# Kernel optimization log

Measured on AMD Instinct MI355X. Metric: run time of the kernel, lower is better.

## Reference

```python
import jax, jax.numpy as jnp
import numpy as np

B, S, D, H = 4, 2048, 1024, 16
HS = D // H  # head_size = 64


def setup_inputs() -> dict:
    key = jax.random.key(0)
    ks = jax.random.split(key, 6)
    scale = 1.0 / np.sqrt(D)
    return {
        "x": jax.random.normal(ks[0], (B, S, D), dtype=jnp.float32),
        "Wk": jax.random.normal(ks[1], (D, D), dtype=jnp.float32) * scale,
        "Wq": jax.random.normal(ks[2], (D, D), dtype=jnp.float32) * scale,
        "Wv": jax.random.normal(ks[3], (D, D), dtype=jnp.float32) * scale,
        "Wo": jax.random.normal(ks[4], (D, D), dtype=jnp.float32) * scale,
        "bo": jnp.zeros((D,), dtype=jnp.float32),
    }


def reference(x, Wk, Wq, Wv, Wo, bo):
    b, s, d = x.shape
    # torch nn.Linear: y = x @ W.T
    def heads(W):
        return (x @ W.T).reshape(b, s, H, HS).transpose(0, 2, 1, 3)  # [b,h,s,hs]
    k, q, v = heads(Wk), heads(Wq), heads(Wv)
    att = jnp.einsum("bhqd,bhkd->bhqk", q, k) * (1.0 / np.sqrt(HS))
    causal = jnp.tril(jnp.ones((s, s), dtype=bool))
    att = jnp.where(causal, att, -jnp.inf)
    att = jax.nn.softmax(att, axis=-1)
    # dropout in eval mode (identity) for deterministic reference
    out = jnp.einsum("bhqk,bhkd->bhqd", att, v)  # [b,h,s,hs]
    out = out.transpose(0, 2, 1, 3).reshape(b, s, d)
    return out @ Wo.T + bo
```

## Files before the change

kernel.cpp:

```cpp
#include <hip/hip_runtime.h>

#define B_ 4
#define S_ 2048
#define D_ 1024
#define H_ 16
#define HS_ 64

typedef float f32x4 __attribute__((ext_vector_type(4)));
typedef short bf16x8 __attribute__((ext_vector_type(8)));

__device__ inline short f2bf(float f) {
  union { float f; unsigned u; } v; v.f = f;
  unsigned r = v.u + 0x7fffu + ((v.u >> 16) & 1u);
  return (short)(r >> 16);
}
__device__ inline unsigned fbits(float f) {
  union { float f; unsigned u; } v; v.f = f; return v.u;
}

__device__ inline void load_lds16(const short* g, short* l) {
  __builtin_amdgcn_global_load_lds((const __attribute__((address_space(1))) void*)g,
                                   (__attribute__((address_space(3))) void*)l, 16, 0, 0);
}

__global__ __launch_bounds__(256) void cvt_f32_bf16(const float* __restrict__ in,
                                                    short* __restrict__ out, int n) {
  const int i = (blockIdx.x * 256 + threadIdx.x) * 4;
  if (i < n) {
    const float4 v = *(const float4*)(in + i);
    short4 o;
    o.x = f2bf(v.x); o.y = f2bf(v.y); o.z = f2bf(v.z); o.w = f2bf(v.w);
    *(short4*)(out + i) = o;
  }
}

__global__ __launch_bounds__(256) void cvt4_f32_bf16(const float* __restrict__ w0, const float* __restrict__ w1,
                                                     const float* __restrict__ w2, const float* __restrict__ w3,
                                                     short* __restrict__ o0, short* __restrict__ o1,
                                                     short* __restrict__ o2, short* __restrict__ o3, int n) {
  const float* in; short* out;
  switch (blockIdx.y) {
    case 0: in = w0; out = o0; break;
    case 1: in = w1; out = o1; break;
    case 2: in = w2; out = o2; break;
    default: in = w3; out = o3; break;
  }
  const int i = (blockIdx.x * 256 + threadIdx.x) * 4;
  if (i < n) {
    const float4 v = *(const float4*)(in + i);
    short4 o;
    o.x = f2bf(v.x); o.y = f2bf(v.y); o.z = f2bf(v.z); o.w = f2bf(v.w);
    *(short4*)(out + i) = o;
  }
}

__device__ inline void stage_tile64(const short* __restrict__ g, int ld, int k0,
                                    short* l, int tid) {
  const int srow = tid >> 3;
  const int scol = (tid & 7) * 8;
  const int scg  = ((tid & 7) ^ ((tid >> 3) & 7)) * 8;
  for (int j = 0; j < 4; j++)
    load_lds16(&g[(size_t)(srow + j * 32) * ld + k0 + scg], &l[(srow + j * 32) * 64 + scol]);
}

__device__ inline void mfma_core64(const short* lA, const short* lB, int wm, int wn,
                                   int col, int quad, f32x4 acc[4][4]) {
  for (int ks = 0; ks < 2; ks++) {
    const int cs = ((ks * 4 + quad) ^ (col & 7)) * 8;
    bf16x8 af[4], bfr[4];
    for (int i = 0; i < 4; i++) af[i]  = *(const bf16x8*)&lA[(wm + i * 16 + col) * 64 + cs];
    for (int j = 0; j < 4; j++) bfr[j] = *(const bf16x8*)&lB[(wn + j * 16 + col) * 64 + cs];
    for (int i = 0; i < 4; i++)
      for (int j = 0; j < 4; j++)
        acc[i][j] = __builtin_amdgcn_mfma_f32_16x16x32_bf16(af[i], bfr[j], acc[i][j], 0, 0, 0);
  }
}

template <bool CF32>
__global__ __launch_bounds__(256) void gemm_bb(const short* __restrict__ A,
                                               const short* __restrict__ Bt,
                                               void* __restrict__ Cv,
                                               const float* __restrict__ bias,
                                               int M, int N, int K) {
  __shared__ __align__(16) short lA[2][128 * 64];
  __shared__ __align__(16) short lB[2][128 * 64];
  const int tid = threadIdx.x;
  const int wave = tid >> 6, lane = tid & 63;
  const int quad = lane >> 4, col = lane & 15;
  const int m0 = blockIdx.x * 128, n0 = blockIdx.y * 128;
  const int wm = (wave >> 1) * 64, wn = (wave & 1) * 64;

  f32x4 acc[4][4];
  for (int i = 0; i < 4; i++)
    for (int j = 0; j < 4; j++) acc[i][j] = (f32x4){0.f, 0.f, 0.f, 0.f};

  const int NT = K >> 6;
  stage_tile64(&A[(size_t)m0 * K], K, 0, lA[0], tid);
  stage_tile64(&Bt[(size_t)n0 * K], K, 0, lB[0], tid);
  __syncthreads();
  for (int kt = 0; kt < NT; kt++) {
    const int cur = kt & 1;
    if (kt + 1 < NT) {
      stage_tile64(&A[(size_t)m0 * K], K, (kt + 1) * 64, lA[cur ^ 1], tid);
      stage_tile64(&Bt[(size_t)n0 * K], K, (kt + 1) * 64, lB[cur ^ 1], tid);
    }
    mfma_core64(lA[cur], lB[cur], wm, wn, col, quad, acc);
    __syncthreads();
  }

  for (int j = 0; j < 4; j++) {
    const int gn = n0 + wn + j * 16 + col;
    const float bv = bias ? bias[gn] : 0.f;
    for (int i = 0; i < 4; i++) {
      const int gm = m0 + wm + i * 16 + quad * 4;
      for (int r = 0; r < 4; r++) {
        if (CF32) ((float*)Cv)[(size_t)(gm + r) * N + gn] = acc[i][j][r] + bv;
        else      ((short*)Cv)[(size_t)(gm + r) * N + gn] = f2bf(acc[i][j][r] + bv);
      }
    }
  }
}

__global__ __launch_bounds__(512, 2) void gemm_qkv8(const short* __restrict__ A,
                                                    const short* Wq, const short* Wk, const short* Wv,
                                                    short* Cq, short* Ck, short* Cvt) {
  __shared__ __align__(16) short lds[3][24576];
  const int tid = threadIdx.x;
  const int wave = tid >> 6, lane = tid & 63;
  const int quad = lane >> 4, col = lane & 15;
  const int nsel = blockIdx.y >> 2;
  const int n0 = (blockIdx.y & 3) * 256;
  const short* Bt = nsel == 0 ? Wq : (nsel == 1 ? Wk : Wv);
  const int m0 = blockIdx.x * 128;
  const int wm = (wave >> 2) * 64, wn = (wave & 3) * 64;
  const int K = D_;
  const int NT = 16;

  const int srow = tid >> 3;
  const int sc8 = tid & 7;
  const short* gA = &A[(size_t)m0 * K];
  const short* gB = &Bt[(size_t)n0 * K];

  auto stageA = [&](int t, int p) {
    const int row = p * 64 + srow;
    load_lds16(&gA[(size_t)row * K + t * 64 + ((sc8 ^ (row & 7)) * 8)],
               &lds[t % 3][row * 64 + sc8 * 8]);
  };
  auto stageB = [&](int t, int p) {
    const int row = p * 64 + srow;
    load_lds16(&gB[(size_t)row * K + t * 64 + ((sc8 ^ (row & 7)) * 8)],
               &lds[t % 3][8192 + row * 64 + sc8 * 8]);
  };

  f32x4 acc[4][4];
#pragma unroll
  for (int i = 0; i < 4; i++)
#pragma unroll
    for (int j = 0; j < 4; j++) acc[i][j] = (f32x4){0.f, 0.f, 0.f, 0.f};

  stageA(0, 0); stageA(0, 1);
  for (int p = 0; p < 4; p++) stageB(0, p);
  stageA(1, 0); stageA(1, 1);
  for (int p = 0; p < 4; p++) stageB(1, p);
  asm volatile("s_waitcnt vmcnt(6)" ::: "memory");
  __builtin_amdgcn_sched_barrier(0);
  __builtin_amdgcn_s_barrier();

  for (int t = 0; t < NT; t++) {
    const short* la = lds[t % 3];
    const short* lb = la + 8192;

    bf16x8 bfr[4][2];
    {
      bf16x8 af[2][2];
#pragma unroll
      for (int j = 0; j < 4; j++)
#pragma unroll
        for (int kk = 0; kk < 2; kk++)
          bfr[j][kk] = *(const bf16x8*)&lb[(wn + j * 16 + col) * 64 +
                                           (((kk * 4 + quad) ^ (col & 7)) * 8)];
#pragma unroll
      for (int f = 0; f < 2; f++)
#pragma unroll
        for (int kk = 0; kk < 2; kk++)
          af[f][kk] = *(const bf16x8*)&la[(wm + f * 16 + col) * 64 +
                                          (((kk * 4 + quad) ^ (col & 7)) * 8)];
      if (t + 2 < NT) { stageB(t + 2, 0); stageB(t + 2, 1); stageB(t + 2, 2); }
      __builtin_amdgcn_sched_barrier(0);
      __builtin_amdgcn_s_barrier();
      asm volatile("s_waitcnt lgkmcnt(0)" ::: "memory");
      __builtin_amdgcn_sched_barrier(0);
      __builtin_amdgcn_s_setprio(1);
#pragma unroll
      for (int f = 0; f < 2; f++)
#pragma unroll
        for (int j = 0; j < 4; j++)
#pragma unroll
          for (int kk = 0; kk < 2; kk++)
            acc[f][j] = __builtin_amdgcn_mfma_f32_16x16x32_bf16(
                af[f][kk], bfr[j][kk], acc[f][j], 0, 0, 0);
      __builtin_amdgcn_s_setprio(0);
      __builtin_amdgcn_sched_barrier(0);
      __builtin_amdgcn_s_barrier();
    }
    {
      bf16x8 af[2][2];
#pragma unroll
      for (int f = 0; f < 2; f++)
#pragma unroll
        for (int kk = 0; kk < 2; kk++)
          af[f][kk] = *(const bf16x8*)&la[(wm + (2 + f) * 16 + col) * 64 +
                                          (((kk * 4 + quad) ^ (col & 7)) * 8)];
      if (t + 2 < NT) { stageB(t + 2, 3); stageA(t + 2, 0); stageA(t + 2, 1); }
      __builtin_amdgcn_sched_barrier(0);
      __builtin_amdgcn_s_barrier();
      asm volatile("s_waitcnt lgkmcnt(0)" ::: "memory");
      __builtin_amdgcn_sched_barrier(0);
      __builtin_amdgcn_s_setprio(1);
#pragma unroll
      for (int f = 0; f < 2; f++)
#pragma unroll
        for (int j = 0; j < 4; j++)
#pragma unroll
          for (int kk = 0; kk < 2; kk++)
            acc[2 + f][j] = __builtin_amdgcn_mfma_f32_16x16x32_bf16(
                af[f][kk], bfr[j][kk], acc[2 + f][j], 0, 0, 0);
      __builtin_amdgcn_s_setprio(0);
      if (t + 2 < NT)      { asm volatile("s_waitcnt vmcnt(6)" ::: "memory"); }
      else if (t + 1 < NT) { asm volatile("s_waitcnt vmcnt(0)" ::: "memory"); }
      __builtin_amdgcn_sched_barrier(0);
      __builtin_amdgcn_s_barrier();
    }
  }

  if (nsel < 2) {
    short* C = nsel ? Ck : Cq;
    const float sc = nsel == 0 ? 0.18033688f : 1.0f;
    for (int j = 0; j < 4; j++) {
      const int gn = n0 + wn + j * 16 + col;
      for (int i = 0; i < 4; i++) {
        const int gm = m0 + wm + i * 16 + quad * 4;
        for (int r = 0; r < 4; r++)
          C[(size_t)(gm + r) * D_ + gn] = f2bf(acc[i][j][r] * sc);
      }
    }
  } else {
    for (int j = 0; j < 4; j++) {
      const int gn = n0 + wn + j * 16 + col;
      for (int i = 0; i < 4; i++) {
        const int gm = m0 + wm + i * 16 + quad * 4;
        const int bb = gm >> 11, s = gm & 2047;
        short4 o;
        o.x = f2bf(acc[i][j][0]); o.y = f2bf(acc[i][j][1]);
        o.z = f2bf(acc[i][j][2]); o.w = f2bf(acc[i][j][3]);
        *(short4*)&Cvt[((size_t)bb * D_ + gn) * (size_t)S_ + s] = o;
      }
    }
  }
}

__global__ __launch_bounds__(256) void flash_attn6(const short* __restrict__ Q,
                                                   const short* __restrict__ Kt,
                                                   const short* __restrict__ Vt,
                                                   short* __restrict__ O) {
  __shared__ __align__(16) short lK[2][64 * 64];
  __shared__ __align__(16) short lV[2][64 * 64];
  __shared__ __align__(16) short pl[4][16 * 64];
  const int tid = threadIdx.x, wave = tid >> 6, lane = tid & 63;
  const int quad = lane >> 4, col = lane & 15;
  const int bh = blockIdx.x;
  const int b = bh >> 4, h = bh & 15;
  const size_t qkbase = (size_t)b * S_ * D_ + (size_t)h * HS_;
  const size_t vtbase = ((size_t)b * D_ + (size_t)h * HS_) * (size_t)S_;

  const int srow = tid >> 3;
  const int scg = (tid & 7) ^ (srow & 7);
  const int cs0 = (quad ^ (col & 7)) * 8;
  const int cs1 = ((quad + 4) ^ (col & 7)) * 8;
  short* plw = pl[wave];

  bf16x8 ones;
  for (int i = 0; i < 8; i++) ones[i] = (short)0x3F80;

  int nb = 0;

  for (int half = 0; half < 2; half++) {
    const int s = half ? (int)blockIdx.y : 31 - (int)blockIdx.y;
    const int qmin = s * 64 + wave * 16;
    const int L = s;

    load_lds16(&Kt[qkbase + (size_t)srow * D_ + scg * 8],        &lK[nb][tid * 8]);
    load_lds16(&Kt[qkbase + (size_t)(32 + srow) * D_ + scg * 8], &lK[nb][2048 + tid * 8]);
    load_lds16(&Vt[vtbase + (size_t)srow * S_ + scg * 8],        &lV[nb][tid * 8]);
    load_lds16(&Vt[vtbase + (size_t)(srow + 32) * S_ + scg * 8], &lV[nb][2048 + tid * 8]);
    const int cur0 = nb;
    nb ^= 1;

    bf16x8 qf[2];
    for (int x = 0; x < 2; x++)
      qf[x] = *(const bf16x8*)&Q[qkbase + (size_t)(qmin + col) * D_ + x * 32 + quad * 8];

    f32x4 oacc[4], lacc;
    for (int dt = 0; dt < 4; dt++) oacc[dt] = (f32x4){0.f, 0.f, 0.f, 0.f};
    lacc = (f32x4){0.f, 0.f, 0.f, 0.f};

    for (int nt = 0; nt <= L; nt++) {
      const int n0 = nt * 64;
      const int cur = cur0 ^ (nt & 1);
      __syncthreads();
      if (nt < L) {
        const int nn = n0 + 64;
        load_lds16(&Kt[qkbase + (size_t)(nn + srow) * D_ + scg * 8],      &lK[nb][tid * 8]);
        load_lds16(&Kt[qkbase + (size_t)(nn + 32 + srow) * D_ + scg * 8], &lK[nb][2048 + tid * 8]);
        load_lds16(&Vt[vtbase + (size_t)srow * S_ + nn + scg * 8],        &lV[nb][tid * 8]);
        load_lds16(&Vt[vtbase + (size_t)(srow + 32) * S_ + nn + scg * 8], &lV[nb][2048 + tid * 8]);
        nb ^= 1;
      }

      const short* lKc = lK[cur];
      const short* lVc = lV[cur];
      const bool needM = (nt == L);

      bf16x8 kf[4][2];
      for (int t = 0; t < 4; t++) {
        const int rb = (t * 16 + col) * 64;
        kf[t][0] = *(const bf16x8*)&lKc[rb + cs0];
        kf[t][1] = *(const bf16x8*)&lKc[rb + cs1];
      }

      const int qg = qmin + col;
      for (int t = 0; t < 4; t++) {
        f32x4 z = (f32x4){0.f, 0.f, 0.f, 0.f};
        __builtin_amdgcn_s_setprio(1);
        z = __builtin_amdgcn_mfma_f32_16x16x32_bf16(kf[t][0], qf[0], z, 0, 0, 0);
        z = __builtin_amdgcn_mfma_f32_16x16x32_bf16(kf[t][1], qf[1], z, 0, 0, 0);
        __builtin_amdgcn_s_setprio(0);
        float p0 = exp2f(z[0]);
        float p1 = exp2f(z[1]);
        float p2 = exp2f(z[2]);
        float p3 = exp2f(z[3]);
        if (needM) {
          const int kv = n0 + t * 16 + quad * 4;
          if (kv + 0 > qg) p0 = 0.f;
          if (kv + 1 > qg) p1 = 0.f;
          if (kv + 2 > qg) p2 = 0.f;
          if (kv + 3 > qg) p3 = 0.f;
        }
        unsigned d0 = __builtin_amdgcn_perm(fbits(p1), fbits(p0), 0x07060302u);
        unsigned d1 = __builtin_amdgcn_perm(fbits(p3), fbits(p2), 0x07060302u);
        const int cc = (2 * t + (quad >> 1)) ^ (col & 7);
        uint2 w; w.x = d0; w.y = d1;
        *(uint2*)&plw[col * 64 + cc * 8 + (quad & 1) * 4] = w;
      }

      for (int h2 = 0; h2 < 2; h2++) {
        const int cgo = ((h2 * 4 + quad) ^ (col & 7)) * 8;
        const bf16x8 pf = *(const bf16x8*)&plw[col * 64 + cgo];
        bf16x8 vf[4];
        for (int dt = 0; dt < 4; dt++)
          vf[dt] = *(const bf16x8*)&lVc[(dt * 16 + col) * 64 + cgo];
        __builtin_amdgcn_s_setprio(1);
        lacc = __builtin_amdgcn_mfma_f32_16x16x32_bf16(pf, ones, lacc, 0, 0, 0);
        for (int dt = 0; dt < 4; dt++)
          oacc[dt] = __builtin_amdgcn_mfma_f32_16x16x32_bf16(pf, vf[dt], oacc[dt], 0, 0, 0);
        __builtin_amdgcn_s_setprio(0);
      }
    }

    for (int r = 0; r < 4; r++) {
      const float inv = 1.f / lacc[r];
      const size_t row = qkbase + (size_t)(qmin + quad * 4 + r) * D_;
      for (int dt = 0; dt < 4; dt++)
        O[row + dt * 16 + col] = f2bf(oacc[dt][r] * inv);
    }
  }
}

__global__ __launch_bounds__(256) void gemm_ff(const float* __restrict__ A,
                                               const float* __restrict__ Bt,
                                               short* __restrict__ C,
                                               int M, int N, int K) {
  __shared__ __align__(16) short lA[128 * 32];
  __shared__ __align__(16) short lB[128 * 32];
  const int tid = threadIdx.x;
  const int wave = tid >> 6, lane = tid & 63;
  const int quad = lane >> 4, col = lane & 15;
  const int m0 = blockIdx.y * 128, n0 = blockIdx.x * 128;
  const int wm = (wave >> 1) * 64, wn = (wave & 1) * 64;
  const int srow2 = tid >> 1;
  const int sc = (tid & 1) * 16;

  f32x4 acc[4][4];
  for (int i = 0; i < 4; i++)
    for (int j = 0; j < 4; j++) acc[i][j] = (f32x4){0.f, 0.f, 0.f, 0.f};

  for (int k0 = 0; k0 < K; k0 += 32) {
    __syncthreads();
    {
      const float4* ga = (const float4*)&A[(size_t)(m0 + srow2) * K + k0 + sc];
      const float4 v0 = ga[0], v1 = ga[1], v2 = ga[2], v3 = ga[3];
      bf16x8 p0, p1;
      p0[0] = f2bf(v0.x); p0[1] = f2bf(v0.y); p0[2] = f2bf(v0.z); p0[3] = f2bf(v0.w);
      p0[4] = f2bf(v1.x); p0[5] = f2bf(v1.y); p0[6] = f2bf(v1.z); p0[7] = f2bf(v1.w);
      p1[0] = f2bf(v2.x); p1[1] = f2bf(v2.y); p1[2] = f2bf(v2.z); p1[3] = f2bf(v2.w);
      p1[4] = f2bf(v3.x); p1[5] = f2bf(v3.y); p1[6] = f2bf(v3.z); p1[7] = f2bf(v3.w);
      *(bf16x8*)&lA[srow2 * 32 + sc]     = p0;
      *(bf16x8*)&lA[srow2 * 32 + sc + 8] = p1;
    }
    {
      const float4* gb = (const float4*)&Bt[(size_t)(n0 + srow2) * K + k0 + sc];
      const float4 v0 = gb[0], v1 = gb[1], v2 = gb[2], v3 = gb[3];
      bf16x8 p0, p1;
      p0[0] = f2bf(v0.x); p0[1] = f2bf(v0.y); p0[2] = f2bf(v0.z); p0[3] = f2bf(v0.w);
      p0[4] = f2bf(v1.x); p0[5] = f2bf(v1.y); p0[6] = f2bf(v1.z); p0[7] = f2bf(v1.w);
      p1[0] = f2bf(v2.x); p1[1] = f2bf(v2.y); p1[2] = f2bf(v2.z); p1[3] = f2bf(v2.w);
      p1[4] = f2bf(v3.x); p1[5] = f2bf(v3.y); p1[6] = f2bf(v3.z); p1[7] = f2bf(v3.w);
      *(bf16x8*)&lB[srow2 * 32 + sc]     = p0;
      *(bf16x8*)&lB[srow2 * 32 + sc + 8] = p1;
    }
    __syncthreads();
    {
      bf16x8 af[4], bfr[4];
      for (int i = 0; i < 4; i++) af[i]  = *(const bf16x8*)&lA[(wm + i * 16 + col) * 32 + quad * 8];
      for (int j = 0; j < 4; j++) bfr[j] = *(const bf16x8*)&lB[(wn + j * 16 + col) * 32 + quad * 8];
      for (int i = 0; i < 4; i++)
        for (int j = 0; j < 4; j++)
          acc[i][j] = __builtin_amdgcn_mfma_f32_16x16x32_bf16(af[i], bfr[j], acc[i][j], 0, 0, 0);
    }
  }

  for (int j = 0; j < 4; j++) {
    const int gn = n0 + wn + j * 16 + col;
    for (int i = 0; i < 4; i++) {
      const int gm = m0 + wm + i * 16 + quad * 4;
      for (int r = 0; r < 4; r++)
        C[(size_t)(gm + r) * N + gn] = f2bf(acc[i][j][r]);
    }
  }
}

__global__ __launch_bounds__(256) void gemm_out_bf(const short* __restrict__ A,
                                                   const float* __restrict__ Bt,
                                                   float* __restrict__ C,
                                                   const float* __restrict__ bias,
                                                   int M, int N, int K) {
  __shared__ __align__(16) short lA[128 * 32];
  __shared__ __align__(16) short lB[128 * 32];
  const int tid = threadIdx.x;
  const int wave = tid >> 6, lane = tid & 63;
  const int quad = lane >> 4, col = lane & 15;
  const int m0 = blockIdx.y * 128, n0 = blockIdx.x * 128;
  const int wm = (wave >> 1) * 64, wn = (wave & 1) * 64;
  const int srow = wave * 32 + (lane >> 2);
  const int scol = (lane & 3) * 8;
  const int srow2 = tid >> 1;
  const int sc = (tid & 1) * 16;

  f32x4 acc[4][4];
  for (int i = 0; i < 4; i++)
    for (int j = 0; j < 4; j++) acc[i][j] = (f32x4){0.f, 0.f, 0.f, 0.f};

  for (int k0 = 0; k0 < K; k0 += 32) {
    __syncthreads();
    load_lds16(&A[(size_t)(m0 + srow) * K + k0 + scol],      &lA[srow * 32 + scol]);
    load_lds16(&A[(size_t)(m0 + srow + 16) * K + k0 + scol], &lA[(srow + 16) * 32 + scol]);
    {
      const float4* gb = (const float4*)&Bt[(size_t)(n0 + srow2) * K + k0 + sc];
      const float4 v0 = gb[0], v1 = gb[1], v2 = gb[2], v3 = gb[3];
      bf16x8 p0, p1;
      p0[0] = f2bf(v0.x); p0[1] = f2bf(v0.y); p0[2] = f2bf(v0.z); p0[3] = f2bf(v0.w);
      p0[4] = f2bf(v1.x); p0[5] = f2bf(v1.y); p0[6] = f2bf(v1.z); p0[7] = f2bf(v1.w);
      p1[0] = f2bf(v2.x); p1[1] = f2bf(v2.y); p1[2] = f2bf(v2.z); p1[3] = f2bf(v2.w);
      p1[4] = f2bf(v3.x); p1[5] = f2bf(v3.y); p1[6] = f2bf(v3.z); p1[7] = f2bf(v3.w);
      *(bf16x8*)&lB[srow2 * 32 + sc]     = p0;
      *(bf16x8*)&lB[srow2 * 32 + sc + 8] = p1;
    }
    __syncthreads();
    {
      bf16x8 af[4], bfr[4];
      for (int i = 0; i < 4; i++) af[i]  = *(const bf16x8*)&lA[(wm + i * 16 + col) * 32 + quad * 8];
      for (int j = 0; j < 4; j++) bfr[j] = *(const bf16x8*)&lB[(wn + j * 16 + col) * 32 + quad * 8];
      for (int i = 0; i < 4; i++)
        for (int j = 0; j < 4; j++)
          acc[i][j] = __builtin_amdgcn_mfma_f32_16x16x32_bf16(af[i], bfr[j], acc[i][j], 0, 0, 0);
    }
  }

  for (int j = 0; j < 4; j++) {
    const int gn = n0 + wn + j * 16 + col;
    const float bv = bias ? bias[gn] : 0.f;
    for (int i = 0; i < 4; i++) {
      const int gm = m0 + wm + i * 16 + quad * 4;
      for (int r = 0; r < 4; r++)
        C[(size_t)(gm + r) * N + gn] = acc[i][j][r] + bv;
    }
  }
}

__global__ __launch_bounds__(64) void flash_attn(const short* __restrict__ Q,
                                                 const short* __restrict__ K,
                                                 const short* __restrict__ V,
                                                 short* __restrict__ O) {
  __shared__ __align__(16) short pl[16 * 40];
  const int lane = threadIdx.x;
  const int quad = lane >> 4, col = lane & 15;
  const int blk = blockIdx.x;
  const int qt = blk & 127;
  const int bh = blk >> 7;
  const int b = bh >> 4, h = bh & 15;
  const int q0 = qt * 16;
  const size_t base = (size_t)b * S_ * D_ + (size_t)h * HS_;

  const bf16x8 qf0 = *(const bf16x8*)&Q[base + (size_t)(q0 + col) * D_ + quad * 8];
  const bf16x8 qf1 = *(const bf16x8*)&Q[base + (size_t)(q0 + col) * D_ + 32 + quad * 8];

  float mr[4], lr[4];
  f32x4 oacc[4];
  for (int r = 0; r < 4; r++) { mr[r] = -1e30f; lr[r] = 0.f; }
  for (int dt = 0; dt < 4; dt++) oacc[dt] = (f32x4){0.f, 0.f, 0.f, 0.f};

  const int ntiles = (q0 + 15) / 32 + 1;
  for (int nt = 0; nt < ntiles; nt++) {
    const int n0 = nt * 32;
    f32x4 s[2];
    s[0] = (f32x4){0.f, 0.f, 0.f, 0.f};
    s[1] = (f32x4){0.f, 0.f, 0.f, 0.f};
    for (int t = 0; t < 2; t++) {
      const short* kp = &K[base + (size_t)(n0 + t * 16 + col) * D_ + quad * 8];
      const bf16x8 kf0 = *(const bf16x8*)kp;
      const bf16x8 kf1 = *(const bf16x8*)(kp + 32);
      s[t] = __builtin_amdgcn_mfma_f32_16x16x32_bf16(qf0, kf0, s[t], 0, 0, 0);
      s[t] = __builtin_amdgcn_mfma_f32_16x16x32_bf16(qf1, kf1, s[t], 0, 0, 0);
    }
    for (int r = 0; r < 4; r++) {
      const int mg = q0 + quad * 4 + r;
      float s0 = s[0][r] * 0.125f; if (n0 + col > mg)      s0 = -1e30f;
      float s1 = s[1][r] * 0.125f; if (n0 + 16 + col > mg) s1 = -1e30f;
      float tm = fmaxf(s0, s1);
      for (int off = 1; off < 16; off <<= 1) tm = fmaxf(tm, __shfl_xor(tm, off));
      const float mnew = fmaxf(mr[r], tm);
      const float alpha = __expf(mr[r] - mnew);
      mr[r] = mnew;
      const float p0 = __expf(s0 - mnew);
      const float p1 = __expf(s1 - mnew);
      float ps = p0 + p1;
      for (int off = 1; off < 16; off <<= 1) ps += __shfl_xor(ps, off);
      lr[r] = lr[r] * alpha + ps;
      for (int dt = 0; dt < 4; dt++) oacc[dt][r] *= alpha;
      pl[(quad * 4 + r) * 40 + col]      = f2bf(p0);
      pl[(quad * 4 + r) * 40 + 16 + col] = f2bf(p1);
    }
    const bf16x8 pf = *(const bf16x8*)&pl[col * 40 + quad * 8];
    for (int dt = 0; dt < 4; dt++) {
      bf16x8 vf;
      const short* vp = &V[base + (size_t)(n0 + quad * 8) * D_ + dt * 16 + col];
      for (int j = 0; j < 8; j++) vf[j] = vp[(size_t)j * D_];
      oacc[dt] = __builtin_amdgcn_mfma_f32_16x16x32_bf16(pf, vf, oacc[dt], 0, 0, 0);
    }
  }

  for (int r = 0; r < 4; r++) {
    const float inv = 1.f / lr[r];
    const size_t row = base + (size_t)(q0 + quad * 4 + r) * D_;
    for (int dt = 0; dt < 4; dt++)
      O[row + dt * 16 + col] = f2bf(oacc[dt][r] * inv);
  }
}

extern "C" void kernel_launch(void* const* d_in, const int* in_sizes, int n_in,
                              void* d_out, int out_size, void* d_ws, size_t ws_size,
                              hipStream_t stream) {
  const float* x  = (const float*)d_in[0];
  const float* Wk = (const float*)d_in[1];
  const float* Wq = (const float*)d_in[2];
  const float* Wv = (const float*)d_in[3];
  const float* Wo = (const float*)d_in[4];
  const float* bo = (const float*)d_in[5];
  float* out = (float*)d_out;

  char* ws = (char*)d_ws;
  const size_t MiB = 1u << 20;
  const int M = B_ * S_, N = D_, K = D_;
  const int nx = M * D_, nw = D_ * D_;

  if (ws_size >= 88 * MiB) {
    short* xb    = (short*)(ws);
    short* wkb   = (short*)(ws + 16 * MiB);
    short* wqb   = (short*)(ws + 18 * MiB);
    short* wvb   = (short*)(ws + 20 * MiB);
    short* wob   = (short*)(ws + 22 * MiB);
    short* q_ws  = (short*)(ws + 24 * MiB);
    short* k_ws  = (short*)(ws + 40 * MiB);
    short* vt_ws = (short*)(ws + 56 * MiB);
    short* a_ws  = (short*)(ws + 72 * MiB);

    hipLaunchKernelGGL(cvt_f32_bf16, dim3(nx / 1024), dim3(256), 0, stream, x, xb, nx);
    hipLaunchKernelGGL(cvt4_f32_bf16, dim3(nw / 1024, 4), dim3(256), 0, stream,
                       Wq, Wk, Wv, Wo, wqb, wkb, wvb, wob, nw);
    hipLaunchKernelGGL(gemm_qkv8, dim3(M / 128, 12), dim3(512), 0, stream,
                       xb, wqb, wkb, wvb, q_ws, k_ws, vt_ws);
    hipLaunchKernelGGL(flash_attn6, dim3(B_ * H_, 16), dim3(256), 0, stream,
                       q_ws, k_ws, vt_ws, a_ws);
    hipLaunchKernelGGL((gemm_bb<true>), dim3(M / 128, N / 128), dim3(256), 0, stream,
                       a_ws, wob, (void*)out, bo, M, N, K);
  } else if (ws_size >= 64 * MiB) {
    short* q_ws = (short*)(ws);
    short* k_ws = (short*)(ws + 16 * MiB);
    short* v_ws = (short*)(ws + 32 * MiB);
    short* a_ws = (short*)(ws + 48 * MiB);
    dim3 gg(N / 128, M / 128), gb(256);
    hipLaunchKernelGGL(gemm_ff, gg, gb, 0, stream, x, Wq, q_ws, M, N, K);
    hipLaunchKernelGGL(gemm_ff, gg, gb, 0, stream, x, Wk, k_ws, M, N, K);
    hipLaunchKernelGGL(gemm_ff, gg, gb, 0, stream, x, Wv, v_ws, M, N, K);
    hipLaunchKernelGGL(flash_attn, dim3(B_ * H_ * (S_ / 16)), dim3(64), 0, stream, q_ws, k_ws, v_ws, a_ws);
    hipLaunchKernelGGL(gemm_out_bf, gg, gb, 0, stream, a_ws, Wo, out, bo, M, N, K);
  } else {
    short* q_ws = (short*)(ws);
    short* k_ws = (short*)(ws + 4 * MiB);
    short* v_ws = (short*)(ws + 8 * MiB);
    short* a_ws = (short*)(ws + 12 * MiB);
    const int Mb = S_;
    dim3 gg(N / 128, Mb / 128), gb(256);
    for (int b = 0; b < B_; b++) {
      const float* xb = x + (size_t)b * S_ * D_;
      float* ob = out + (size_t)b * S_ * D_;
      hipLaunchKernelGGL(gemm_ff, gg, gb, 0, stream, xb, Wq, q_ws, Mb, N, K);
      hipLaunchKernelGGL(gemm_ff, gg, gb, 0, stream, xb, Wk, k_ws, Mb, N, K);
      hipLaunchKernelGGL(gemm_ff, gg, gb, 0, stream, xb, Wv, v_ws, Mb, N, K);
      hipLaunchKernelGGL(flash_attn, dim3(H_ * (S_ / 16)), dim3(64), 0, stream, q_ws, k_ws, v_ws, a_ws);
      hipLaunchKernelGGL(gemm_out_bf, gg, gb, 0, stream, a_ws, Wo, ob, bo, Mb, N, K);
    }
  }
}
```

Measured before the change: 250.5 us.

## Add 8-wave triple-buffered output GEMM and use raw exp2 intrinsic in attention

Replaces the 256-thread output projection GEMM with a new 512-thread kernel using 128x256 tiles. It triple-buffers LDS via direct global-to-LDS loads, splits each K-step into two halves interleaved with prefetch, and uses explicit waitcnt and barriers. Separately, the attention softmax swaps exp2f for the hardware exp2 intrinsic to drop the library's range handling. The new GEMM uses much more LDS (~144KB) and fewer blocks, which may limit occupancy. The raw exp2 may differ slightly for denormal inputs.

```diff
diff --git a/kernel.cpp b/kernel.cpp
--- a/kernel.cpp
+++ b/kernel.cpp
@@ -17,6 +17,7 @@
 __device__ inline unsigned fbits(float f) {
   union { float f; unsigned u; } v; v.f = f; return v.u;
 }
+__device__ inline float fexp2(float x) { return __builtin_amdgcn_exp2f(x); }
 
 __device__ inline void load_lds16(const short* g, short* l) {
   __builtin_amdgcn_global_load_lds((const __attribute__((address_space(1))) void*)g,
@@ -259,6 +260,128 @@
   }
 }
 
+__global__ __launch_bounds__(512, 2) void gemm_bb8(const short* __restrict__ A,
+                                                   const short* __restrict__ Bt,
+                                                   float* __restrict__ C,
+                                                   const float* __restrict__ bias) {
+  __shared__ __align__(16) short lds[3][24576];
+  const int tid = threadIdx.x;
+  const int wave = tid >> 6, lane = tid & 63;
+  const int quad = lane >> 4, col = lane & 15;
+  const int n0 = blockIdx.y * 256;
+  const int m0 = blockIdx.x * 128;
+  const int wm = (wave >> 2) * 64, wn = (wave & 3) * 64;
+  const int K = D_, N = D_;
+  const int NT = 16;
+
+  const int srow = tid >> 3;
+  const int sc8 = tid & 7;
+  const short* gA = &A[(size_t)m0 * K];
+  const short* gB = &Bt[(size_t)n0 * K];
+
+  auto stageA = [&](int t, int p) {
+    const int row = p * 64 + srow;
+    load_lds16(&gA[(size_t)row * K + t * 64 + ((sc8 ^ (row & 7)) * 8)],
+               &lds[t % 3][row * 64 + sc8 * 8]);
+  };
+  auto stageB = [&](int t, int p) {
+    const int row = p * 64 + srow;
+    load_lds16(&gB[(size_t)row * K + t * 64 + ((sc8 ^ (row & 7)) * 8)],
+               &lds[t % 3][8192 + row * 64 + sc8 * 8]);
+  };
+
+  f32x4 acc[4][4];
+#pragma unroll
+  for (int i = 0; i < 4; i++)
+#pragma unroll
+    for (int j = 0; j < 4; j++) acc[i][j] = (f32x4){0.f, 0.f, 0.f, 0.f};
+
+  stageA(0, 0); stageA(0, 1);
+  for (int p = 0; p < 4; p++) stageB(0, p);
+  stageA(1, 0); stageA(1, 1);
+  for (int p = 0; p < 4; p++) stageB(1, p);
+  asm volatile("s_waitcnt vmcnt(6)" ::: "memory");
+  __builtin_amdgcn_sched_barrier(0);
+  __builtin_amdgcn_s_barrier();
+
+  for (int t = 0; t < NT; t++) {
+    const short* la = lds[t % 3];
+    const short* lb = la + 8192;
+
+    bf16x8 bfr[4][2];
+    {
+      bf16x8 af[2][2];
+#pragma unroll
+      for (int j = 0; j < 4; j++)
+#pragma unroll
+        for (int kk = 0; kk < 2; kk++)
+          bfr[j][kk] = *(const bf16x8*)&lb[(wn + j * 16 + col) * 64 +
+                                           (((kk * 4 + quad) ^ (col & 7)) * 8)];
+#pragma unroll
+      for (int f = 0; f < 2; f++)
+#pragma unroll
+        for (int kk = 0; kk < 2; kk++)
+          af[f][kk] = *(const bf16x8*)&la[(wm + f * 16 + col) * 64 +
+                                          (((kk * 4 + quad) ^ (col & 7)) * 8)];
+      if (t + 2 < NT) { stageB(t + 2, 0); stageB(t + 2, 1); stageB(t + 2, 2); }
+      __builtin_amdgcn_sched_barrier(0);
+      __builtin_amdgcn_s_barrier();
+      asm volatile("s_waitcnt lgkmcnt(0)" ::: "memory");
+      __builtin_amdgcn_sched_barrier(0);
+      __builtin_amdgcn_s_setprio(1);
+#pragma unroll
+      for (int f = 0; f < 2; f++)
+#pragma unroll
+        for (int j = 0; j < 4; j++)
+#pragma unroll
+          for (int kk = 0; kk < 2; kk++)
+            acc[f][j] = __builtin_amdgcn_mfma_f32_16x16x32_bf16(
+                af[f][kk], bfr[j][kk], acc[f][j], 0, 0, 0);
+      __builtin_amdgcn_s_setprio(0);
+      __builtin_amdgcn_sched_barrier(0);
+      __builtin_amdgcn_s_barrier();
+    }
+    {
+      bf16x8 af[2][2];
+#pragma unroll
+      for (int f = 0; f < 2; f++)
+#pragma unroll
+        for (int kk = 0; kk < 2; kk++)
+          af[f][kk] = *(const bf16x8*)&la[(wm + (2 + f) * 16 + col) * 64 +
+                                          (((kk * 4 + quad) ^ (col & 7)) * 8)];
+      if (t + 2 < NT) { stageB(t + 2, 3); stageA(t + 2, 0); stageA(t + 2, 1); }
+      __builtin_amdgcn_sched_barrier(0);
+      __builtin_amdgcn_s_barrier();
+      asm volatile("s_waitcnt lgkmcnt(0)" ::: "memory");
+      __builtin_amdgcn_sched_barrier(0);
+      __builtin_amdgcn_s_setprio(1);
+#pragma unroll
+      for (int f = 0; f < 2; f++)
+#pragma unroll
+        for (int j = 0; j < 4; j++)
+#pragma unroll
+          for (int kk = 0; kk < 2; kk++)
+            acc[2 + f][j] = __builtin_amdgcn_mfma_f32_16x16x32_bf16(
+                af[f][kk], bfr[j][kk], acc[2 + f][j], 0, 0, 0);
+      __builtin_amdgcn_s_setprio(0);
+      if (t + 2 < NT)      { asm volatile("s_waitcnt vmcnt(6)" ::: "memory"); }
+      else if (t + 1 < NT) { asm volatile("s_waitcnt vmcnt(0)" ::: "memory"); }
+      __builtin_amdgcn_sched_barrier(0);
+      __builtin_amdgcn_s_barrier();
+    }
+  }
+
+  for (int j = 0; j < 4; j++) {
+    const int gn = n0 + wn + j * 16 + col;
+    const float bv = bias[gn];
+    for (int i = 0; i < 4; i++) {
+      const int gm = m0 + wm + i * 16 + quad * 4;
+      for (int r = 0; r < 4; r++)
+        C[(size_t)(gm + r) * N + gn] = acc[i][j][r] + bv;
+    }
+  }
+}
+
 __global__ __launch_bounds__(256) void flash_attn6(const short* __restrict__ Q,
                                                    const short* __restrict__ Kt,
                                                    const short* __restrict__ Vt,
@@ -335,10 +458,10 @@
         z = __builtin_amdgcn_mfma_f32_16x16x32_bf16(kf[t][0], qf[0], z, 0, 0, 0);
         z = __builtin_amdgcn_mfma_f32_16x16x32_bf16(kf[t][1], qf[1], z, 0, 0, 0);
         __builtin_amdgcn_s_setprio(0);
-        float p0 = exp2f(z[0]);
-        float p1 = exp2f(z[1]);
-        float p2 = exp2f(z[2]);
-        float p3 = exp2f(z[3]);
+        float p0 = fexp2(z[0]);
+        float p1 = fexp2(z[1]);
+        float p2 = fexp2(z[2]);
+        float p3 = fexp2(z[3]);
         if (needM) {
           const int kv = n0 + t * 16 + quad * 4;
           if (kv + 0 > qg) p0 = 0.f;
@@ -601,8 +724,8 @@
                        xb, wqb, wkb, wvb, q_ws, k_ws, vt_ws);
     hipLaunchKernelGGL(flash_attn6, dim3(B_ * H_, 16), dim3(256), 0, stream,
                        q_ws, k_ws, vt_ws, a_ws);
-    hipLaunchKernelGGL((gemm_bb<true>), dim3(M / 128, N / 128), dim3(256), 0, stream,
-                       a_ws, wob, (void*)out, bo, M, N, K);
+    hipLaunchKernelGGL(gemm_bb8, dim3(M / 128, N / 256), dim3(512), 0, stream,
+                       a_ws, wob, out, bo);
   } else if (ws_size >= 64 * MiB) {
     short* q_ws = (short*)(ws);
     short* k_ws = (short*)(ws + 16 * MiB);
```

Measured after the change: 230.6 us. -7.9%, faster.
